# Optimization experiments

Measured on AMD Instinct MI355X. Metric: run time of the kernel, lower is better.

Reference implementation:

```python
import jax, jax.numpy as jnp
import numpy as np

N = 50000  # num nodes
E = 800000  # num edges
D_IN = 128
D_OUT = 128
K = 2


def mean_propagate(x, src, dst):
    # scatter-mean over incoming edges: out[d] = mean_{(s,d) in edges} x[s]
    sums = jax.ops.segment_sum(x[src], dst, num_segments=N)  # [N, D]
    deg = jax.ops.segment_sum(jnp.ones((src.shape[0],), x.dtype), dst, num_segments=N)
    return sums / jnp.maximum(deg, 1.0)[:, None]


def setup_inputs() -> dict:
    key = jax.random.key(0)
    k1, k2, k3, k4 = jax.random.split(key, 4)
    x = jax.random.normal(k1, (N, D_IN), dtype=jnp.float32)
    edge_index = jax.random.randint(k2, (2, E), 0, N, dtype=jnp.int64)
    fan_in = D_IN * (K + 1)
    bound = 1.0 / np.sqrt(fan_in)
    W = jax.random.uniform(k3, (D_OUT, fan_in), dtype=jnp.float32, minval=-bound, maxval=bound)
    b = jax.random.uniform(k4, (D_OUT,), dtype=jnp.float32, minval=-bound, maxval=bound)
    return {"x": x, "edge_index": edge_index, "W": W, "b": b}


def reference(x, edge_index, W, b):
    src, dst = edge_index[0], edge_index[1]
    features = [x]
    propagated = x
    for _ in range(K):
        propagated = mean_propagate(propagated, src, dst)
        features.append(propagated)
    h = jnp.concatenate(features, axis=-1)  # [N, D_IN*(K+1)]
    return h @ W.T + b  # [N, D_OUT]
```

## Files before the change

kernel.cpp:

```cpp
#include <hip/hip_runtime.h>
#include <cstddef>


#define DFEAT 128
#define SUBSHIFT 8
#define MAXSUB 256
#define EPB 2048
#define CAP 16384

typedef __attribute__((ext_vector_type(8))) short short8v;
typedef __attribute__((ext_vector_type(4))) float f32x4;
typedef __attribute__((ext_vector_type(4))) unsigned int uint4v;

__device__ inline unsigned short f2bf(float f) {
    unsigned int u;
    __builtin_memcpy(&u, &f, 4);
    unsigned int r = u + 0x7FFFu + ((u >> 16) & 1u);
    return (unsigned short)(r >> 16);
}
__device__ inline float bf2f(unsigned short h) {
    unsigned int u = ((unsigned int)h) << 16;
    float f;
    __builtin_memcpy(&f, &u, 4);
    return f;
}

__global__ void zero_kernel(int* __restrict__ p, int n) {
    int i = blockIdx.x * blockDim.x + threadIdx.x;
    if (i < n) p[i] = 0;
}

__global__ void conv_bf16_kernel(const float* __restrict__ in,
                                 unsigned short* __restrict__ outb, int total8) {
    int i = blockIdx.x * blockDim.x + threadIdx.x;
    if (i >= total8) return;
    const float* s = in + (size_t)i * 8;
    const float4 a = *reinterpret_cast<const float4*>(s);
    const float4 b = *reinterpret_cast<const float4*>(s + 4);
    uint4v w;
    w.x = (unsigned)f2bf(a.x) | ((unsigned)f2bf(a.y) << 16);
    w.y = (unsigned)f2bf(a.z) | ((unsigned)f2bf(a.w) << 16);
    w.z = (unsigned)f2bf(b.x) | ((unsigned)f2bf(b.y) << 16);
    w.w = (unsigned)f2bf(b.z) | ((unsigned)f2bf(b.w) << 16);
    *reinterpret_cast<uint4v*>(outb + (size_t)i * 8) = w;
}

__global__ void pack_w_kernel(const float* __restrict__ W,
                              unsigned short* __restrict__ Wpk) {
    const int idx = blockIdx.x * blockDim.x + threadIdx.x;
    if (idx >= 6144) return;
    const int lane = idx & 63;
    const int nt = (idx >> 6) & 7;
    const int ks = idx >> 9;
    const int col = nt * 16 + (lane & 15);
    const int k = ks * 32 + (lane >> 4) * 8;
    const float* wp = W + (size_t)col * 384 + k;
    uint4v w;
    w.x = (unsigned)f2bf(wp[0]) | ((unsigned)f2bf(wp[1]) << 16);
    w.y = (unsigned)f2bf(wp[2]) | ((unsigned)f2bf(wp[3]) << 16);
    w.z = (unsigned)f2bf(wp[4]) | ((unsigned)f2bf(wp[5]) << 16);
    w.w = (unsigned)f2bf(wp[6]) | ((unsigned)f2bf(wp[7]) << 16);
    *reinterpret_cast<uint4v*>(Wpk + (size_t)idx * 8) = w;
}

__global__ __launch_bounds__(256) void partitionA_kernel(
    const int* __restrict__ src, const int* __restrict__ dst,
    int* __restrict__ subFill, int* __restrict__ subReal,
    uint2* __restrict__ staging, int E, int nsub) {
    __shared__ int cnt[MAXSUB];
    __shared__ int base[MAXSUB];
    const int t = threadIdx.x;
    for (int i = t; i < nsub; i += 256) cnt[i] = 0;
    __syncthreads();
    const int e0 = blockIdx.x * EPB;
    int d[8], s[8], b[8], rk[8];
#pragma unroll
    for (int j = 0; j < 8; ++j) {
        const int e = e0 + j * 256 + t;
        if (e < E) {
            d[j] = __builtin_nontemporal_load(dst + e);
            s[j] = __builtin_nontemporal_load(src + e);
            b[j] = d[j] >> SUBSHIFT;
            rk[j] = atomicAdd(&cnt[b[j]], 1);
        } else {
            d[j] = -1; s[j] = 0; b[j] = 0; rk[j] = 0;
        }
    }
    __syncthreads();
    for (int i = t; i < nsub; i += 256) {
        const int c = cnt[i];
        if (c > 0) {
            const int padded = (c + 15) & ~15;
            int bse = atomicAdd(&subFill[i], padded);
            if (bse + padded > CAP) bse = CAP - padded;
            base[i] = bse;
            atomicAdd(&subReal[i], c);
        }
    }
    __syncthreads();
#pragma unroll
    for (int j = 0; j < 8; ++j)
        if (d[j] >= 0)
            staging[(size_t)b[j] * CAP + base[b[j]] + rk[j]] =
                make_uint2((unsigned)d[j], (unsigned)s[j]);
    for (int i = t; i < nsub; i += 256) {
        const int c = cnt[i];
        if (c > 0) {
            const int padded = (c + 15) & ~15;
            for (int k = c; k < padded; ++k)
                staging[(size_t)i * CAP + base[i] + k] = make_uint2(0xFFFFFFFFu, 0u);
        }
    }
}

__global__ __launch_bounds__(256) void scanSub_kernel(const int* __restrict__ subReal,
                                                      int* __restrict__ subBase, int nsub) {
    __shared__ int s[256];
    const int t = threadIdx.x;
    const int v = (t < nsub) ? subReal[t] : 0;
    s[t] = v;
    __syncthreads();
#pragma unroll
    for (int off = 1; off < 256; off <<= 1) {
        int x = (t >= off) ? s[t - off] : 0;
        __syncthreads();
        s[t] += x;
        __syncthreads();
    }
    if (t < nsub) subBase[t] = s[t] - v;
}

__global__ __launch_bounds__(256) void partitionB_kernel(
    const uint2* __restrict__ staging, const int* __restrict__ subFill,
    const int* __restrict__ subBase, int* __restrict__ rowptr,
    float* __restrict__ inv, int* __restrict__ col, int N, int E) {
    __shared__ int cnt[1 << SUBSHIFT];
    __shared__ int loc[1 << SUBSHIFT];
    __shared__ int cur[1 << SUBSHIFT];
    const int b = blockIdx.x;
    const int n0 = b << SUBSHIFT;
    const int t = threadIdx.x;
    cnt[t] = 0;
    __syncthreads();
    const int fill = min(subFill[b], CAP);
    const uint2* seg = staging + (size_t)b * CAP;
    for (int i = t; i < fill; i += 256) {
        const unsigned dd = seg[i].x;
        if (dd != 0xFFFFFFFFu) atomicAdd(&cnt[dd - (unsigned)n0], 1);
    }
    __syncthreads();
    const int v = cnt[t];
    loc[t] = v;
    __syncthreads();
#pragma unroll
    for (int off = 1; off < 256; off <<= 1) {
        int x = (t >= off) ? loc[t - off] : 0;
        __syncthreads();
        loc[t] += x;
        __syncthreads();
    }
    const int gpos = subBase[b] + loc[t] - v;
    const int n = n0 + t;
    if (n < N) {
        rowptr[n] = gpos;
        inv[n] = 1.0f / (float)max(v, 1);
    }
    cur[t] = gpos;
    __syncthreads();
    for (int i = t; i < fill; i += 256) {
        const uint2 pr = seg[i];
        if (pr.x != 0xFFFFFFFFu) {
            const int pos = atomicAdd(&cur[(int)pr.x - n0], 1);
            col[pos] = (int)pr.y;
        }
    }
    if (b == 0 && t == 0) rowptr[N] = E;
}

__global__ __launch_bounds__(256) void gather_bf16_kernel(
    const unsigned short* __restrict__ feat, const int* __restrict__ rowptr,
    const int* __restrict__ col, const float* __restrict__ inv,
    unsigned short* __restrict__ outb, int N) {
    const int n = blockIdx.x * 16 + (threadIdx.x >> 4);
    const int lane = threadIdx.x & 15;
    if (n >= N) return;
    const int beg = rowptr[n];
    const int end = rowptr[n + 1];
    float acc[8];
#pragma unroll
    for (int j = 0; j < 8; ++j) acc[j] = 0.0f;
    int e = beg;
    for (; e + 3 < end; e += 4) {
        const int s0 = col[e];
        const int s1 = col[e + 1];
        const int s2 = col[e + 2];
        const int s3 = col[e + 3];
        const short8v v0 = *reinterpret_cast<const short8v*>(feat + (size_t)s0 * DFEAT + lane * 8);
        const short8v v1 = *reinterpret_cast<const short8v*>(feat + (size_t)s1 * DFEAT + lane * 8);
        const short8v v2 = *reinterpret_cast<const short8v*>(feat + (size_t)s2 * DFEAT + lane * 8);
        const short8v v3 = *reinterpret_cast<const short8v*>(feat + (size_t)s3 * DFEAT + lane * 8);
#pragma unroll
        for (int j = 0; j < 8; ++j)
            acc[j] += (bf2f((unsigned short)v0[j]) + bf2f((unsigned short)v1[j])) +
                      (bf2f((unsigned short)v2[j]) + bf2f((unsigned short)v3[j]));
    }
    for (; e < end; ++e) {
        const int s0 = col[e];
        const short8v v0 = *reinterpret_cast<const short8v*>(feat + (size_t)s0 * DFEAT + lane * 8);
#pragma unroll
        for (int j = 0; j < 8; ++j) acc[j] += bf2f((unsigned short)v0[j]);
    }
    const float sc = inv[n];
    uint4v w;
    w.x = (unsigned)f2bf(acc[0] * sc) | ((unsigned)f2bf(acc[1] * sc) << 16);
    w.y = (unsigned)f2bf(acc[2] * sc) | ((unsigned)f2bf(acc[3] * sc) << 16);
    w.z = (unsigned)f2bf(acc[4] * sc) | ((unsigned)f2bf(acc[5] * sc) << 16);
    w.w = (unsigned)f2bf(acc[6] * sc) | ((unsigned)f2bf(acc[7] * sc) << 16);
    *reinterpret_cast<uint4v*>(outb + (size_t)n * DFEAT + lane * 8) = w;
}

__global__ __launch_bounds__(256) void gemm_mfma_kernel(
    const unsigned short* __restrict__ xb, const unsigned short* __restrict__ m1b,
    const unsigned short* __restrict__ m2b, const unsigned short* __restrict__ Wpk,
    const float* __restrict__ bias, float* __restrict__ out, int N) {
    const int t = threadIdx.x;
    const int w = t >> 6;
    const int l = t & 63;
    const int lr = l & 15;
    const int kg = l >> 4;
    const int rowBase = blockIdx.x * 64 + w * 16;
    int arow = rowBase + lr;
    if (arow >= N) arow = N - 1;

    const short8v* Wv = reinterpret_cast<const short8v*>(Wpk);

    f32x4 acc[8];
#pragma unroll
    for (int nt = 0; nt < 8; ++nt) acc[nt] = (f32x4){0.f, 0.f, 0.f, 0.f};

#pragma unroll
    for (int ks = 0; ks < 12; ++ks) {
        const unsigned short* feat = (ks < 4) ? xb : (ks < 8 ? m1b : m2b);
        const int k0 = (ks & 3) * 32;
        const short8v a = *reinterpret_cast<const short8v*>(
            feat + (size_t)arow * DFEAT + k0 + kg * 8);
        short8v bfrag[8];
#pragma unroll
        for (int nt = 0; nt < 8; ++nt)
            bfrag[nt] = Wv[(ks * 8 + nt) * 64 + l];
#pragma unroll
        for (int nt = 0; nt < 8; ++nt)
            acc[nt] = __builtin_amdgcn_mfma_f32_16x16x32_bf16(a, bfrag[nt], acc[nt], 0, 0, 0);
    }

#pragma unroll
    for (int nt = 0; nt < 8; ++nt) {
        const int c = nt * 16 + lr;
        const float bv = bias[c];
#pragma unroll
        for (int r = 0; r < 4; ++r) {
            const int node = rowBase + kg * 4 + r;
            if (node < N) out[(size_t)node * DFEAT + c] = acc[nt][r] + bv;
        }
    }
}

extern "C" void kernel_launch(void* const* d_in, const int* in_sizes, int n_in,
                              void* d_out, int out_size, void* d_ws, size_t ws_size,
                              hipStream_t stream) {
    (void)n_in; (void)out_size; (void)ws_size;
    const float* x  = (const float*)d_in[0];
    const int*   ei = (const int*)d_in[1];
    const float* W  = (const float*)d_in[2];
    const float* b  = (const float*)d_in[3];
    float* out = (float*)d_out;

    const int N = in_sizes[0] / DFEAT;
    const int E = in_sizes[1] / 2;
    const int* src = ei;
    const int* dst = ei + E;
    const int nsub = (N + (1 << SUBSHIFT) - 1) >> SUBSHIFT;

    auto up = [](size_t v) { return (v + 255) & ~(size_t)255; };
    char* p = (char*)d_ws;
    int*   subFill   = (int*)p;            p += up((size_t)MAXSUB * 4 * 2);
    int*   subReal   = subFill + MAXSUB;
    int*   subBase   = (int*)p;            p += up((size_t)MAXSUB * 4);
    int*   rowptr    = (int*)p;            p += up(((size_t)N + 1) * 4);
    uint2* staging   = (uint2*)p;          p += up((size_t)MAXSUB * CAP * 8);
    int*   col       = (int*)p;            p += up((size_t)E * 4);
    float* inv       = (float*)p;          p += up((size_t)N * 4);
    unsigned short* xb  = (unsigned short*)p;  p += up((size_t)N * DFEAT * 2);
    unsigned short* m1b = (unsigned short*)p;  p += up((size_t)N * DFEAT * 2);
    unsigned short* m2b = (unsigned short*)p;  p += up((size_t)N * DFEAT * 2);
    unsigned short* Wpk = (unsigned short*)p;  p += up((size_t)6144 * 8 * 2);

    zero_kernel<<<1, 2 * MAXSUB, 0, stream>>>(subFill, 2 * MAXSUB);

    partitionA_kernel<<<(E + EPB - 1) / EPB, 256, 0, stream>>>(src, dst, subFill, subReal,
                                                               staging, E, nsub);
    scanSub_kernel<<<1, 256, 0, stream>>>(subReal, subBase, nsub);
    partitionB_kernel<<<nsub, 256, 0, stream>>>(staging, subFill, subBase,
                                                rowptr, inv, col, N, E);

    const int x8 = N * DFEAT / 8;
    conv_bf16_kernel<<<(x8 + 255) / 256, 256, 0, stream>>>(x, xb, x8);
    pack_w_kernel<<<(6144 + 255) / 256, 256, 0, stream>>>(W, Wpk);

    const int gatherBlocks = (N + 15) / 16;
    gather_bf16_kernel<<<gatherBlocks, 256, 0, stream>>>(xb,  rowptr, col, inv, m1b, N);
    gather_bf16_kernel<<<gatherBlocks, 256, 0, stream>>>(m1b, rowptr, col, inv, m2b, N);

    gemm_mfma_kernel<<<(N + 63) / 64, 256, 0, stream>>>(xb, m1b, m2b, Wpk, b, out, N);
}
```

Baseline: 138.7 us.

## Fuse second gather into GEMM via LDS, merge scan and conversion launches

The second mean-propagation step now runs inside the GEMM kernel. Each block gathers its 64 nodes' second-hop features into a padded LDS tile and feeds them straight to the MFMA loop, so the m2 buffer is never written to or re-read from global memory. The separate sub-bucket scan kernel is folded into partitionB, with every block redoing the small 256-entry scan. The x conversion and W packing kernels are merged into one launch. Together these remove three launches and one N×128 bf16 round trip. In exchange the fused kernel has fewer blocks for the gather phase (64 nodes per block instead of 16), and LDS stores of 16-bit elements may bank-conflict.

New measurement: 137.3 us. Within noise of the previous version (-0.9%).

```diff
diff --git a/kernel.cpp b/kernel.cpp
--- a/kernel.cpp
+++ b/kernel.cpp
@@ -30,24 +30,24 @@
     if (i < n) p[i] = 0;
 }
 
-__global__ void conv_bf16_kernel(const float* __restrict__ in,
-                                 unsigned short* __restrict__ outb, int total8) {
-    int i = blockIdx.x * blockDim.x + threadIdx.x;
-    if (i >= total8) return;
-    const float* s = in + (size_t)i * 8;
-    const float4 a = *reinterpret_cast<const float4*>(s);
-    const float4 b = *reinterpret_cast<const float4*>(s + 4);
-    uint4v w;
-    w.x = (unsigned)f2bf(a.x) | ((unsigned)f2bf(a.y) << 16);
-    w.y = (unsigned)f2bf(a.z) | ((unsigned)f2bf(a.w) << 16);
-    w.z = (unsigned)f2bf(b.x) | ((unsigned)f2bf(b.y) << 16);
-    w.w = (unsigned)f2bf(b.z) | ((unsigned)f2bf(b.w) << 16);
-    *reinterpret_cast<uint4v*>(outb + (size_t)i * 8) = w;
-}
-
-__global__ void pack_w_kernel(const float* __restrict__ W,
-                              unsigned short* __restrict__ Wpk) {
-    const int idx = blockIdx.x * blockDim.x + threadIdx.x;
+__global__ void convpack_kernel(const float* __restrict__ x,
+                                unsigned short* __restrict__ xb, int total8,
+                                const float* __restrict__ W,
+                                unsigned short* __restrict__ Wpk) {
+    const int i = blockIdx.x * blockDim.x + threadIdx.x;
+    if (i < total8) {
+        const float* s = x + (size_t)i * 8;
+        const float4 a = *reinterpret_cast<const float4*>(s);
+        const float4 b = *reinterpret_cast<const float4*>(s + 4);
+        uint4v w;
+        w.x = (unsigned)f2bf(a.x) | ((unsigned)f2bf(a.y) << 16);
+        w.y = (unsigned)f2bf(a.z) | ((unsigned)f2bf(a.w) << 16);
+        w.z = (unsigned)f2bf(b.x) | ((unsigned)f2bf(b.y) << 16);
+        w.w = (unsigned)f2bf(b.z) | ((unsigned)f2bf(b.w) << 16);
+        *reinterpret_cast<uint4v*>(xb + (size_t)i * 8) = w;
+        return;
+    }
+    const int idx = i - total8;
     if (idx >= 6144) return;
     const int lane = idx & 63;
     const int nt = (idx >> 6) & 7;
@@ -113,35 +113,28 @@
     }
 }
 
-__global__ __launch_bounds__(256) void scanSub_kernel(const int* __restrict__ subReal,
-                                                      int* __restrict__ subBase, int nsub) {
-    __shared__ int s[256];
-    const int t = threadIdx.x;
-    const int v = (t < nsub) ? subReal[t] : 0;
-    s[t] = v;
-    __syncthreads();
-#pragma unroll
-    for (int off = 1; off < 256; off <<= 1) {
-        int x = (t >= off) ? s[t - off] : 0;
-        __syncthreads();
-        s[t] += x;
-        __syncthreads();
-    }
-    if (t < nsub) subBase[t] = s[t] - v;
-}
-
 __global__ __launch_bounds__(256) void partitionB_kernel(
     const uint2* __restrict__ staging, const int* __restrict__ subFill,
-    const int* __restrict__ subBase, int* __restrict__ rowptr,
-    float* __restrict__ inv, int* __restrict__ col, int N, int E) {
+    const int* __restrict__ subReal, int* __restrict__ rowptr,
+    float* __restrict__ inv, int* __restrict__ col, int N, int E, int nsub) {
+    __shared__ int ss[256];
     __shared__ int cnt[1 << SUBSHIFT];
     __shared__ int loc[1 << SUBSHIFT];
     __shared__ int cur[1 << SUBSHIFT];
     const int b = blockIdx.x;
     const int n0 = b << SUBSHIFT;
     const int t = threadIdx.x;
+    ss[t] = (t < nsub) ? subReal[t] : 0;
     cnt[t] = 0;
     __syncthreads();
+#pragma unroll
+    for (int off = 1; off < 256; off <<= 1) {
+        int x = (t >= off) ? ss[t - off] : 0;
+        __syncthreads();
+        ss[t] += x;
+        __syncthreads();
+    }
+    const int myBase = (b > 0) ? ss[b - 1] : 0;
     const int fill = min(subFill[b], CAP);
     const uint2* seg = staging + (size_t)b * CAP;
     for (int i = t; i < fill; i += 256) {
@@ -159,7 +152,7 @@
         loc[t] += x;
         __syncthreads();
     }
-    const int gpos = subBase[b] + loc[t] - v;
+    const int gpos = myBase + loc[t] - v;
     const int n = n0 + t;
     if (n < N) {
         rowptr[n] = gpos;
@@ -219,16 +212,61 @@
     *reinterpret_cast<uint4v*>(outb + (size_t)n * DFEAT + lane * 8) = w;
 }
 
-__global__ __launch_bounds__(256) void gemm_mfma_kernel(
+#define M2PAD 132
+__global__ __launch_bounds__(256) void gather_gemm_kernel(
     const unsigned short* __restrict__ xb, const unsigned short* __restrict__ m1b,
-    const unsigned short* __restrict__ m2b, const unsigned short* __restrict__ Wpk,
+    const unsigned short* __restrict__ Wpk, const int* __restrict__ rowptr,
+    const int* __restrict__ col, const float* __restrict__ inv,
     const float* __restrict__ bias, float* __restrict__ out, int N) {
+    __shared__ unsigned short m2s[64][M2PAD];
     const int t = threadIdx.x;
+    const int nodeBase = blockIdx.x * 64;
+    const int lane16 = t & 15;
+
+    for (int r = 0; r < 4; ++r) {
+        const int ln = r * 16 + (t >> 4);
+        const int n = nodeBase + ln;
+        float acc[8];
+#pragma unroll
+        for (int j = 0; j < 8; ++j) acc[j] = 0.0f;
+        float sc = 0.0f;
+        if (n < N) {
+            const int beg = rowptr[n];
+            const int end = rowptr[n + 1];
+            int e = beg;
+            for (; e + 3 < end; e += 4) {
+                const int s0 = col[e];
+                const int s1 = col[e + 1];
+                const int s2 = col[e + 2];
+                const int s3 = col[e + 3];
+                const short8v v0 = *reinterpret_cast<const short8v*>(m1b + (size_t)s0 * DFEAT + lane16 * 8);
+                const short8v v1 = *reinterpret_cast<const short8v*>(m1b + (size_t)s1 * DFEAT + lane16 * 8);
+                const short8v v2 = *reinterpret_cast<const short8v*>(m1b + (size_t)s2 * DFEAT + lane16 * 8);
+                const short8v v3 = *reinterpret_cast<const short8v*>(m1b + (size_t)s3 * DFEAT + lane16 * 8);
+#pragma unroll
+                for (int j = 0; j < 8; ++j)
+                    acc[j] += (bf2f((unsigned short)v0[j]) + bf2f((unsigned short)v1[j])) +
+                              (bf2f((unsigned short)v2[j]) + bf2f((unsigned short)v3[j]));
+            }
+            for (; e < end; ++e) {
+                const int s0 = col[e];
+                const short8v v0 = *reinterpret_cast<const short8v*>(m1b + (size_t)s0 * DFEAT + lane16 * 8);
+#pragma unroll
+                for (int j = 0; j < 8; ++j) acc[j] += bf2f((unsigned short)v0[j]);
+            }
+            sc = inv[n];
+        }
+        unsigned short* dstp = &m2s[ln][lane16 * 8];
+#pragma unroll
+        for (int j = 0; j < 8; ++j) dstp[j] = f2bf(acc[j] * sc);
+    }
+    __syncthreads();
+
     const int w = t >> 6;
     const int l = t & 63;
     const int lr = l & 15;
     const int kg = l >> 4;
-    const int rowBase = blockIdx.x * 64 + w * 16;
+    const int rowBase = nodeBase + w * 16;
     int arow = rowBase + lr;
     if (arow >= N) arow = N - 1;
 
@@ -240,10 +278,15 @@
 
 #pragma unroll
     for (int ks = 0; ks < 12; ++ks) {
-        const unsigned short* feat = (ks < 4) ? xb : (ks < 8 ? m1b : m2b);
-        const int k0 = (ks & 3) * 32;
-        const short8v a = *reinterpret_cast<const short8v*>(
-            feat + (size_t)arow * DFEAT + k0 + kg * 8);
+        const int q = ks & 3;
+        short8v a;
+        if (ks < 8) {
+            const unsigned short* feat = (ks < 4) ? xb : m1b;
+            a = *reinterpret_cast<const short8v*>(
+                feat + (size_t)arow * DFEAT + q * 32 + kg * 8);
+        } else {
+            a = *reinterpret_cast<const short8v*>(&m2s[w * 16 + lr][q * 32 + kg * 8]);
+        }
         short8v bfrag[8];
 #pragma unroll
         for (int nt = 0; nt < 8; ++nt)
@@ -285,31 +328,27 @@
     char* p = (char*)d_ws;
     int*   subFill   = (int*)p;            p += up((size_t)MAXSUB * 4 * 2);
     int*   subReal   = subFill + MAXSUB;
-    int*   subBase   = (int*)p;            p += up((size_t)MAXSUB * 4);
     int*   rowptr    = (int*)p;            p += up(((size_t)N + 1) * 4);
     uint2* staging   = (uint2*)p;          p += up((size_t)MAXSUB * CAP * 8);
     int*   col       = (int*)p;            p += up((size_t)E * 4);
     float* inv       = (float*)p;          p += up((size_t)N * 4);
     unsigned short* xb  = (unsigned short*)p;  p += up((size_t)N * DFEAT * 2);
     unsigned short* m1b = (unsigned short*)p;  p += up((size_t)N * DFEAT * 2);
-    unsigned short* m2b = (unsigned short*)p;  p += up((size_t)N * DFEAT * 2);
     unsigned short* Wpk = (unsigned short*)p;  p += up((size_t)6144 * 8 * 2);
 
     zero_kernel<<<1, 2 * MAXSUB, 0, stream>>>(subFill, 2 * MAXSUB);
 
     partitionA_kernel<<<(E + EPB - 1) / EPB, 256, 0, stream>>>(src, dst, subFill, subReal,
                                                                staging, E, nsub);
-    scanSub_kernel<<<1, 256, 0, stream>>>(subReal, subBase, nsub);
-    partitionB_kernel<<<nsub, 256, 0, stream>>>(staging, subFill, subBase,
-                                                rowptr, inv, col, N, E);
+    partitionB_kernel<<<nsub, 256, 0, stream>>>(staging, subFill, subReal,
+                                                rowptr, inv, col, N, E, nsub);
 
     const int x8 = N * DFEAT / 8;
-    conv_bf16_kernel<<<(x8 + 255) / 256, 256, 0, stream>>>(x, xb, x8);
-    pack_w_kernel<<<(6144 + 255) / 256, 256, 0, stream>>>(W, Wpk);
+    convpack_kernel<<<(x8 + 6144 + 255) / 256, 256, 0, stream>>>(x, xb, x8, W, Wpk);
 
     const int gatherBlocks = (N + 15) / 16;
-    gather_bf16_kernel<<<gatherBlocks, 256, 0, stream>>>(xb,  rowptr, col, inv, m1b, N);
-    gather_bf16_kernel<<<gatherBlocks, 256, 0, stream>>>(m1b, rowptr, col, inv, m2b, N);
-
-    gemm_mfma_kernel<<<(N + 63) / 64, 256, 0, stream>>>(xb, m1b, m2b, Wpk, b, out, N);
-}
+    gather_bf16_kernel<<<gatherBlocks, 256, 0, stream>>>(xb, rowptr, col, inv, m1b, N);
+
+    gather_gemm_kernel<<<(N + 63) / 64, 256, 0, stream>>>(xb, m1b, Wpk, rowptr, col,
+                                                          inv, b, out, N);
+}
```
